# Kernel tuning notes

Hardware: AMD Instinct MI355X
Metric: run time of the kernel (lower is better)

The kernel has to match this reference:

```python
import jax, jax.numpy as jnp
import numpy as np

E = 384      # embed_dim
H = 8        # num_heads
D = E // H   # head_dim = 48
G = 16       # grid_size
HT = 128     # height
WD = 128     # width
FF = 1536
B = 8
EPS = 1e-5


def _ln(x, g, b):
    m = jnp.mean(x, axis=-1, keepdims=True)
    v = jnp.mean(jnp.square(x - m), axis=-1, keepdims=True)
    return (x - m) * jax.lax.rsqrt(v + EPS) * g + b


def _grid_attention(xn, in_proj_w, in_proj_b, out_w, out_b):
    # xn: [B, S, E] with S = HT*WD. Extract 16x16 windows -> [Wn, B, T, E]
    nh, nw = HT // G, WD // G
    T = G * G
    xw = xn.reshape(B, nh, G, nw, G, E).transpose(1, 3, 0, 2, 4, 5)
    xw = xw.reshape(nh * nw, B, T, E)  # [Wn, B, T, E]
    # torch in_proj: qkv = x @ W.T + b, W: [3E, E]
    qkv = jnp.einsum('wbte,fe->wbtf', xw, in_proj_w) + in_proj_b
    q, k, v = jnp.split(qkv, 3, axis=-1)
    q = q.reshape(nh * nw, B, T, H, D)
    k = k.reshape(nh * nw, B, T, H, D)
    v = v.reshape(nh * nw, B, T, H, D)
    scale = 1.0 / jnp.sqrt(jnp.asarray(D, dtype=xn.dtype))
    # NOTE: torch MHA (batch_first=False) treats dim0 of (B, T, E) as seq len,
    # so attention mixes across the batch axis (length B) per window position.
    scores = jnp.einsum('wbtnd,wctnd->wtnbc', q, k) * scale  # [Wn,T,H,B,B]
    p = jax.nn.softmax(scores, axis=-1)
    o = jnp.einsum('wtnbc,wctnd->wbtnd', p, v).reshape(nh * nw, B, T, E)
    o = jnp.einsum('wbte,fe->wbtf', o, out_w) + out_b
    # reassemble windows back to [B, S, E]
    o = o.reshape(nh, nw, B, G, G, E).transpose(2, 0, 3, 1, 4, 5)
    return o.reshape(B, HT * WD, E)


def setup_inputs() -> dict:
    key = jax.random.key(0)
    ks = jax.random.split(key, 6)
    S = HT * WD
    return {
        'x': jax.random.normal(ks[0], (B, S, E), jnp.float32),
        'in_proj_w': jax.random.normal(ks[1], (3 * E, E), jnp.float32) * 0.02,
        'in_proj_b': jnp.zeros((3 * E,), jnp.float32),
        'out_w': jax.random.normal(ks[2], (E, E), jnp.float32) * 0.02,
        'out_b': jnp.zeros((E,), jnp.float32),
        'ln1_g': jnp.ones((E,), jnp.float32),
        'ln1_b': jnp.zeros((E,), jnp.float32),
        'ln2_g': jnp.ones((E,), jnp.float32),
        'ln2_b': jnp.zeros((E,), jnp.float32),
        'w1': jax.random.normal(ks[3], (FF, E), jnp.float32) * 0.02,
        'b1': jnp.zeros((FF,), jnp.float32),
        'w2': jax.random.normal(ks[4], (E, FF), jnp.float32) * 0.02,
        'b2': jnp.zeros((E,), jnp.float32),
    }


def reference(x, in_proj_w, in_proj_b, out_w, out_b, ln1_g, ln1_b,
              ln2_g, ln2_b, w1, b1, w2, b2):
    # Pre-attn LN, windowed MHA (eval mode: dropout off), residual
    attn = _grid_attention(_ln(x, ln1_g, ln1_b), in_proj_w, in_proj_b, out_w, out_b)
    x = x + attn
    # LN + GELU MLP (exact erf gelu, torch nn.GELU default) + residual
    h = _ln(x, ln2_g, ln2_b)
    h = jax.nn.gelu(jnp.einsum('bse,fe->bsf', h, w1) + b1, approximate=False)
    h = jnp.einsum('bsf,ef->bse', h, w2) + b2
    return x + h
```

## Files before the change

### kernel.cpp

```cpp
#include <hip/hip_runtime.h>
#include <hip/hip_bf16.h>
#include <math.h>

typedef unsigned short u16;
typedef __attribute__((ext_vector_type(8))) short short8;
typedef __attribute__((ext_vector_type(4))) float floatx4;

__device__ __forceinline__ float bf2f(u16 u) {
  union { unsigned int i; float f; } w; w.i = ((unsigned int)u) << 16; return w.f;
}
__device__ __forceinline__ u16 f2bf(float f) {
  union { float f; unsigned int i; } w; w.f = f;
  unsigned int r = (w.i + 0x7fffu + ((w.i >> 16) & 1u)) >> 16;
  return (u16)r;
}

__global__ void detect_k(const unsigned int* __restrict__ xw, int* __restrict__ flag) {
  __shared__ int cnt;
  if (threadIdx.x == 0) cnt = 0;
  __syncthreads();
  int c = 0;
  for (int i = threadIdx.x; i < 4096; i += 256) {
    const unsigned int e = (xw[i] >> 7) & 0xffu;
    c += (e >= 0x71u && e <= 0x81u) ? 1 : 0;
  }
  atomicAdd(&cnt, c);
  __syncthreads();
  if (threadIdx.x == 0) flag[0] = (cnt > 2048) ? 1 : 0;
}

__global__ void conv_k(const void* __restrict__ src, u16* __restrict__ dst, int n,
                       const int* __restrict__ flagp) {
  const int dt = flagp[0];
  const int stride = gridDim.x * blockDim.x;
  for (int i = blockIdx.x * blockDim.x + threadIdx.x; i < n; i += stride)
    dst[i] = dt ? ((const u16*)src)[i] : f2bf(((const float*)src)[i]);
}

#define BM 128
#define BN 128
#define BK 64

template<int MODE>
__global__ __launch_bounds__(256, 2) void gemm_bt(
    const u16* __restrict__ A, const u16* __restrict__ Bt,
    const u16* __restrict__ bias, const void* res,
    void* C, int M, int N, int K, int s0, int lsc, int jump,
    const int* __restrict__ flagp)
{
  __shared__ __align__(16) u16 lA[BM * BK];
  __shared__ __align__(16) u16 lB[BN * BK];
  const int tid  = threadIdx.x;
  const int lane = tid & 63;
  const int w    = tid >> 6;
  const int wm   = (w & 1) * 64;
  const int wn   = (w >> 1) * 64;
  const long mbase = (long)blockIdx.x * BM;
  const long nbase = (long)blockIdx.y * BN;
  const int dt = (MODE == 1) ? flagp[0] : 0;

  {
    int4 z; z.x = z.y = z.z = z.w = 0;
    for (int i = tid; i < BM * BK / 8; i += 256) ((int4*)lA)[i] = z;
    for (int i = tid; i < BN * BK / 8; i += 256) ((int4*)lB)[i] = z;
  }
  __syncthreads();

  floatx4 acc[4][4] = {};

  const int srow = w * 32 + (lane >> 3);
  const int kgp  = lane & 7;
  const int frm  = lane & 15;
  const int fkg  = lane >> 4;

  for (int k0 = 0; k0 < K; k0 += BK) {
    #pragma unroll
    for (int j = 0; j < 4; ++j) {
      const int r  = srow + j * 8;
      const int kg = kgp ^ (r & 7);
      const u16* gp = A + (mbase + r) * (long)K + (k0 + kg * 8);
      __builtin_amdgcn_global_load_lds(
          (const __attribute__((address_space(1))) void*)gp,
          (__attribute__((address_space(3))) void*)(lA + (w * 32 + j * 8) * BK),
          16, 0, 0);
    }
    #pragma unroll
    for (int j = 0; j < 4; ++j) {
      const int r  = srow + j * 8;
      const int kg = kgp ^ (r & 7);
      const u16* gp = Bt + (nbase + r) * (long)K + (k0 + kg * 8);
      __builtin_amdgcn_global_load_lds(
          (const __attribute__((address_space(1))) void*)gp,
          (__attribute__((address_space(3))) void*)(lB + (w * 32 + j * 8) * BK),
          16, 0, 0);
    }
    __syncthreads();

    short8 af[2][4], bfr[2][4];
    #pragma unroll
    for (int t = 0; t < 2; ++t) {
      #pragma unroll
      for (int i = 0; i < 4; ++i) {
        const int rm  = wm + i * 16 + frm;
        const int kgd = t * 4 + fkg;
        af[t][i]  = *(const short8*)(lA + rm * BK + ((kgd ^ (rm & 7)) * 8));
        const int rn  = wn + i * 16 + frm;
        bfr[t][i] = *(const short8*)(lB + rn * BK + ((kgd ^ (rn & 7)) * 8));
      }
    }
    #pragma unroll
    for (int t = 0; t < 2; ++t)
      #pragma unroll
      for (int i = 0; i < 4; ++i)
        #pragma unroll
        for (int n = 0; n < 4; ++n)
          acc[i][n] = __builtin_amdgcn_mfma_f32_16x16x32_bf16(
              af[t][i], bfr[t][n], acc[i][n], 0, 0, 0);
    __syncthreads();
  }

  float bv[4];
  #pragma unroll
  for (int n = 0; n < 4; ++n)
    bv[n] = bf2f(bias[nbase + wn + n * 16 + frm]);

  #pragma unroll
  for (int i = 0; i < 4; ++i) {
    #pragma unroll
    for (int n = 0; n < 4; ++n) {
      const long col = nbase + wn + n * 16 + frm;
      #pragma unroll
      for (int r4 = 0; r4 < 4; ++r4) {
        const long row = mbase + wm + i * 16 + (lane >> 4) * 4 + r4;
        float v = acc[i][n][r4] + bv[n];
        if (MODE == 2) v = 0.5f * v * (1.f + erff(v * 0.70710678118654752f));
        if (MODE == 1) {
          const long g   = row + s0 + ((row >> lsc) * (long)jump);
          const long idx = g * (long)N + col;
          if (dt) { v += bf2f(((const u16*)res)[idx]); ((u16*)C)[idx] = f2bf(v); }
          else    { v += ((const float*)res)[idx];     ((float*)C)[idx] = v;     }
        } else {
          ((u16*)C)[row * (long)N + col] = f2bf(v);
        }
      }
    }
  }
}

__global__ __launch_bounds__(256) void ln_k(
    const void* __restrict__ xin, const u16* __restrict__ g,
    const u16* __restrict__ b, u16* __restrict__ y,
    int s0, int lsc, int jump, const int* __restrict__ flagp)
{
  const int dt   = flagp[0];
  const int lane = threadIdx.x & 63;
  const int wv   = threadIdx.x >> 6;
  const long r   = (long)blockIdx.x * 4 + wv;
  const long gr  = r + s0 + ((r >> lsc) * (long)jump);
  float v[6];
  float s = 0.f;
  if (dt) {
    const u16* xp = (const u16*)xin + gr * 384;
    #pragma unroll
    for (int j = 0; j < 3; ++j) {
      const unsigned int u = *(const unsigned int*)(xp + lane * 2 + 128 * j);
      v[2 * j]     = bf2f((u16)(u & 0xffffu));
      v[2 * j + 1] = bf2f((u16)(u >> 16));
      s += v[2 * j] + v[2 * j + 1];
    }
  } else {
    const float* xf = (const float*)xin + gr * 384;
    #pragma unroll
    for (int j = 0; j < 3; ++j) {
      const float2 ld = *(const float2*)(xf + lane * 2 + 128 * j);
      v[2 * j] = ld.x; v[2 * j + 1] = ld.y;
      s += ld.x + ld.y;
    }
  }
  #pragma unroll
  for (int o = 32; o; o >>= 1) s += __shfl_xor(s, o, 64);
  const float mean = s * (1.f / 384.f);
  float vs = 0.f;
  #pragma unroll
  for (int j = 0; j < 6; ++j) { const float d = v[j] - mean; vs += d * d; }
  #pragma unroll
  for (int o = 32; o; o >>= 1) vs += __shfl_xor(vs, o, 64);
  const float rstd = rsqrtf(vs * (1.f / 384.f) + 1e-5f);
  u16* yp = y + r * 384;
  #pragma unroll
  for (int j = 0; j < 3; ++j) {
    const int e = lane * 2 + 128 * j;
    const float o0 = (v[2 * j]     - mean) * rstd * bf2f(g[e])     + bf2f(b[e]);
    const float o1 = (v[2 * j + 1] - mean) * rstd * bf2f(g[e + 1]) + bf2f(b[e + 1]);
    *(unsigned int*)(yp + e) = (unsigned int)f2bf(o0) | ((unsigned int)f2bf(o1) << 16);
  }
}

__global__ __launch_bounds__(512) void attn_k(
    const u16* __restrict__ qkv, u16* __restrict__ o, int sc)
{
  __shared__ __align__(16) u16 sm[8 * 1160];
  const int tid = threadIdx.x;
  const int sl = blockIdx.x;
  for (int u = tid; u < 1152; u += 512) {
    const int b   = u / 144;
    const int c16 = u - b * 144;
    const int4 val = *(const int4*)(qkv + ((size_t)(b * sc + sl)) * 1152 + c16 * 8);
    *(int4*)(sm + b * 1160 + c16 * 8) = val;
  }
  __syncthreads();
  const int lane = tid & 63;
  const int h = tid >> 6;
  const int b = lane >> 3;
  const int c = lane & 7;
  const u16* qrow = sm + b * 1160 + h * 48;
  const u16* krow = sm + c * 1160 + 384 + h * 48;
  float scv = 0.f;
  #pragma unroll
  for (int dd = 0; dd < 6; ++dd) {
    const short8 q8 = *(const short8*)(qrow + dd * 8);
    const short8 k8 = *(const short8*)(krow + dd * 8);
    #pragma unroll
    for (int e = 0; e < 8; ++e)
      scv += bf2f((u16)q8[e]) * bf2f((u16)k8[e]);
  }
  scv *= 0.14433756729740643f;
  float mx = scv;
  mx = fmaxf(mx, __shfl_xor(mx, 1, 64));
  mx = fmaxf(mx, __shfl_xor(mx, 2, 64));
  mx = fmaxf(mx, __shfl_xor(mx, 4, 64));
  const float ex = expf(scv - mx);
  float sum = ex;
  sum += __shfl_xor(sum, 1, 64);
  sum += __shfl_xor(sum, 2, 64);
  sum += __shfl_xor(sum, 4, 64);
  const float p = ex / sum;
  float pc[8];
  #pragma unroll
  for (int cc = 0; cc < 8; ++cc) pc[cc] = __shfl(p, (b << 3) | cc, 64);
  if (c < 6) {
    const int dg = c;
    float oacc[8] = {0, 0, 0, 0, 0, 0, 0, 0};
    #pragma unroll
    for (int cc = 0; cc < 8; ++cc) {
      const short8 v8 = *(const short8*)(sm + cc * 1160 + 768 + h * 48 + dg * 8);
      #pragma unroll
      for (int e = 0; e < 8; ++e) oacc[e] += pc[cc] * bf2f((u16)v8[e]);
    }
    short8 rv;
    #pragma unroll
    for (int e = 0; e < 8; ++e) rv[e] = (short)f2bf(oacc[e]);
    *(short8*)(o + ((size_t)(b * sc + sl)) * 384 + h * 48 + dg * 8) = rv;
  }
}

extern "C" void kernel_launch(void* const* d_in, const int* in_sizes, int n_in,
                              void* d_out, int out_size, void* d_ws, size_t ws_size,
                              hipStream_t stream) {
  (void)in_sizes; (void)n_in; (void)out_size;
  int* flag = (int*)d_ws;
  u16* W    = (u16*)d_ws + 16;
  static const int woff[12] = {0, 442368, 443520, 590976, 591360, 591744,
                               592128, 592512, 592896, 1182720, 1184256, 1774080};
  static const int wlen[12] = {442368, 1152, 147456, 384, 384, 384,
                               384, 384, 589824, 1536, 589824, 384};
  u16* SCR = W + 1774464;
  const size_t used = (size_t)((char*)SCR - (char*)d_ws);
  const size_t avail = (ws_size > used) ? (ws_size - used) : 0;

  detect_k<<<1, 256, 0, stream>>>((const unsigned int*)d_in[0], flag);
  for (int i = 0; i < 12; ++i) {
    const int n  = wlen[i];
    const int nb = (n + 1023) / 1024;
    conv_k<<<(nb < 512 ? nb : 512), 256, 0, stream>>>(d_in[i + 1], W + woff[i], n, flag);
  }
  const u16 *ipw = W + woff[0], *ipb = W + woff[1], *outw = W + woff[2],
            *outb = W + woff[3], *l1g = W + woff[4], *l1b = W + woff[5],
            *l2g = W + woff[6], *l2b = W + woff[7], *w1 = W + woff[8],
            *b1 = W + woff[9], *w2 = W + woff[10], *b2 = W + woff[11];
  const void* x = d_in[0];

  int sc = 16384;
  while (sc > 16 && (size_t)24576 * (size_t)sc > avail) sc >>= 1;
  const int lsc  = 31 - __builtin_clz((unsigned)sc);
  const int jump = 16384 - sc;
  u16* QKV = SCR;
  u16* XO  = QKV + (size_t)9216 * sc;

  for (int c = 0; c < 16384 / sc; ++c) {
    const int s0 = c * sc;
    const int Mc = 8 * sc;
    ln_k<<<Mc / 4, 256, 0, stream>>>(x, l1g, l1b, XO, s0, lsc, jump, flag);
    gemm_bt<0><<<dim3(Mc / 128, 9), 256, 0, stream>>>(
        XO, ipw, ipb, nullptr, QKV, Mc, 1152, 384, 0, 0, 0, flag);
    attn_k<<<sc, 512, 0, stream>>>(QKV, XO, sc);
    gemm_bt<1><<<dim3(Mc / 128, 3), 256, 0, stream>>>(
        XO, outw, outb, x, d_out, Mc, 384, 384, s0, lsc, jump, flag);
  }

  long Mt = (long)(avail / 3840);
  Mt &= ~127L;
  if (Mt > 131072) Mt = 131072;
  if (Mt < 128)    Mt = 128;
  u16* Hb = SCR;
  u16* H1 = Hb + (size_t)Mt * 384;

  for (long t0 = 0; t0 < 131072; t0 += Mt) {
    const int Mtc = (int)((131072 - t0 < Mt) ? (131072 - t0) : Mt);
    ln_k<<<Mtc / 4, 256, 0, stream>>>(d_out, l2g, l2b, Hb, (int)t0, 30, 0, flag);
    gemm_bt<2><<<dim3(Mtc / 128, 12), 256, 0, stream>>>(
        Hb, w1, b1, nullptr, H1, Mtc, 1536, 384, 0, 0, 0, flag);
    gemm_bt<1><<<dim3(Mtc / 128, 3), 256, 0, stream>>>(
        H1, w2, b2, d_out, d_out, Mtc, 384, 1536, (int)t0, 30, 0, flag);
  }
}
```

Before: 1.796 ms.

## Double-buffer GEMM LDS tiles, enlarge M tile, add XCD-aware block swizzle

Result: slower. 2.042 ms (+13.7%).

```diff
diff --git a/kernel.cpp b/kernel.cpp
--- a/kernel.cpp
+++ b/kernel.cpp
@@ -37,65 +37,69 @@
     dst[i] = dt ? ((const u16*)src)[i] : f2bf(((const float*)src)[i]);
 }
 
-#define BM 128
+#define BM 256
 #define BN 128
 #define BK 64
 
 template<int MODE>
-__global__ __launch_bounds__(256, 2) void gemm_bt(
+__global__ __launch_bounds__(512, 2) void gemm_bt(
     const u16* __restrict__ A, const u16* __restrict__ Bt,
     const u16* __restrict__ bias, const void* res,
     void* C, int M, int N, int K, int s0, int lsc, int jump,
     const int* __restrict__ flagp)
 {
-  __shared__ __align__(16) u16 lA[BM * BK];
-  __shared__ __align__(16) u16 lB[BN * BK];
+  __shared__ __align__(16) u16 lA[2][BM * BK];
+  __shared__ __align__(16) u16 lB[2][BN * BK];
   const int tid  = threadIdx.x;
   const int lane = tid & 63;
   const int w    = tid >> 6;
-  const int wm   = (w & 1) * 64;
-  const int wn   = (w >> 1) * 64;
-  const long mbase = (long)blockIdx.x * BM;
-  const long nbase = (long)blockIdx.y * BN;
+  const int wm   = (w >> 1) * 64;
+  const int wn   = (w & 1) * 64;
+
+  const int nbn = N / BN;
+  const int nwg = gridDim.x;
+  const int q = nwg >> 3, r = nwg & 7;
+  const int xcd = blockIdx.x & 7, lid = blockIdx.x >> 3;
+  const int gid = (xcd < r ? xcd * (q + 1) : r * (q + 1) + (xcd - r) * q) + lid;
+  const long mbase = (long)(gid / nbn) * BM;
+  const long nbase = (long)(gid % nbn) * BN;
   const int dt = (MODE == 1) ? flagp[0] : 0;
 
-  {
-    int4 z; z.x = z.y = z.z = z.w = 0;
-    for (int i = tid; i < BM * BK / 8; i += 256) ((int4*)lA)[i] = z;
-    for (int i = tid; i < BN * BK / 8; i += 256) ((int4*)lB)[i] = z;
-  }
-  __syncthreads();
-
   floatx4 acc[4][4] = {};
 
-  const int srow = w * 32 + (lane >> 3);
-  const int kgp  = lane & 7;
-  const int frm  = lane & 15;
-  const int fkg  = lane >> 4;
-
-  for (int k0 = 0; k0 < K; k0 += BK) {
+  const int srow8 = lane >> 3;
+  const int kgp   = lane & 7;
+  const int frm   = lane & 15;
+  const int fkg   = lane >> 4;
+
+  const int nk = K / BK;
+
+  auto STAGE = [&](int buf, int k0) {
     #pragma unroll
     for (int j = 0; j < 4; ++j) {
-      const int r  = srow + j * 8;
-      const int kg = kgp ^ (r & 7);
-      const u16* gp = A + (mbase + r) * (long)K + (k0 + kg * 8);
+      const int rr = w * 32 + j * 8;
+      const int rA = rr + srow8;
+      const int kg = kgp ^ (rA & 7);
+      const u16* gp = A + (mbase + rA) * (long)K + (k0 + kg * 8);
       __builtin_amdgcn_global_load_lds(
           (const __attribute__((address_space(1))) void*)gp,
-          (__attribute__((address_space(3))) void*)(lA + (w * 32 + j * 8) * BK),
+          (__attribute__((address_space(3))) void*)(&lA[buf][rr * BK]),
           16, 0, 0);
     }
     #pragma unroll
-    for (int j = 0; j < 4; ++j) {
-      const int r  = srow + j * 8;
-      const int kg = kgp ^ (r & 7);
-      const u16* gp = Bt + (nbase + r) * (long)K + (k0 + kg * 8);
+    for (int j = 0; j < 2; ++j) {
+      const int rr = w * 16 + j * 8;
+      const int rB = rr + srow8;
+      const int kg = kgp ^ (rB & 7);
+      const u16* gp = Bt + (nbase + rB) * (long)K + (k0 + kg * 8);
       __builtin_amdgcn_global_load_lds(
           (const __attribute__((address_space(1))) void*)gp,
-          (__attribute__((address_space(3))) void*)(lB + (w * 32 + j * 8) * BK),
+          (__attribute__((address_space(3))) void*)(&lB[buf][rr * BK]),
           16, 0, 0);
     }
-    __syncthreads();
-
+  };
+
+  auto COMPUTE = [&](int buf) {
     short8 af[2][4], bfr[2][4];
     #pragma unroll
     for (int t = 0; t < 2; ++t) {
@@ -103,9 +107,9 @@
       for (int i = 0; i < 4; ++i) {
         const int rm  = wm + i * 16 + frm;
         const int kgd = t * 4 + fkg;
-        af[t][i]  = *(const short8*)(lA + rm * BK + ((kgd ^ (rm & 7)) * 8));
+        af[t][i]  = *(const short8*)(&lA[buf][rm * BK + ((kgd ^ (rm & 7)) * 8)]);
         const int rn  = wn + i * 16 + frm;
-        bfr[t][i] = *(const short8*)(lB + rn * BK + ((kgd ^ (rn & 7)) * 8));
+        bfr[t][i] = *(const short8*)(&lB[buf][rn * BK + ((kgd ^ (rn & 7)) * 8)]);
       }
     }
     #pragma unroll
@@ -116,8 +120,18 @@
         for (int n = 0; n < 4; ++n)
           acc[i][n] = __builtin_amdgcn_mfma_f32_16x16x32_bf16(
               af[t][i], bfr[t][n], acc[i][n], 0, 0, 0);
+  };
+
+  STAGE(0, 0);
+  __syncthreads();
+  int cur = 0;
+  for (int t = 0; t < nk - 1; ++t) {
+    STAGE(cur ^ 1, (t + 1) * BK);
+    COMPUTE(cur);
     __syncthreads();
-  }
+    cur ^= 1;
+  }
+  COMPUTE(cur);
 
   float bv[4];
   #pragma unroll
@@ -281,7 +295,7 @@
   const void* x = d_in[0];
 
   int sc = 16384;
-  while (sc > 16 && (size_t)24576 * (size_t)sc > avail) sc >>= 1;
+  while (sc > 32 && (size_t)24576 * (size_t)sc > avail) sc >>= 1;
   const int lsc  = 31 - __builtin_clz((unsigned)sc);
   const int jump = 16384 - sc;
   u16* QKV = SCR;
@@ -291,26 +305,26 @@
     const int s0 = c * sc;
     const int Mc = 8 * sc;
     ln_k<<<Mc / 4, 256, 0, stream>>>(x, l1g, l1b, XO, s0, lsc, jump, flag);
-    gemm_bt<0><<<dim3(Mc / 128, 9), 256, 0, stream>>>(
+    gemm_bt<0><<<(Mc / 256) * 9, 512, 0, stream>>>(
         XO, ipw, ipb, nullptr, QKV, Mc, 1152, 384, 0, 0, 0, flag);
     attn_k<<<sc, 512, 0, stream>>>(QKV, XO, sc);
-    gemm_bt<1><<<dim3(Mc / 128, 3), 256, 0, stream>>>(
+    gemm_bt<1><<<(Mc / 256) * 3, 512, 0, stream>>>(
         XO, outw, outb, x, d_out, Mc, 384, 384, s0, lsc, jump, flag);
   }
 
   long Mt = (long)(avail / 3840);
-  Mt &= ~127L;
   if (Mt > 131072) Mt = 131072;
-  if (Mt < 128)    Mt = 128;
+  if (Mt < 256)    Mt = 256;
+  while (Mt & (Mt - 1)) Mt &= Mt - 1;
   u16* Hb = SCR;
   u16* H1 = Hb + (size_t)Mt * 384;
 
   for (long t0 = 0; t0 < 131072; t0 += Mt) {
     const int Mtc = (int)((131072 - t0 < Mt) ? (131072 - t0) : Mt);
     ln_k<<<Mtc / 4, 256, 0, stream>>>(d_out, l2g, l2b, Hb, (int)t0, 30, 0, flag);
-    gemm_bt<2><<<dim3(Mtc / 128, 12), 256, 0, stream>>>(
+    gemm_bt<2><<<(Mtc / 256) * 12, 512, 0, stream>>>(
         Hb, w1, b1, nullptr, H1, Mtc, 1536, 384, 0, 0, 0, flag);
-    gemm_bt<1><<<dim3(Mtc / 128, 3), 256, 0, stream>>>(
+    gemm_bt<1><<<(Mtc / 256) * 3, 512, 0, stream>>>(
         H1, w2, b2, d_out, d_out, Mtc, 384, 1536, (int)t0, 30, 0, flag);
   }
 }
```
